# Kernel tuning notes

Hardware: AMD Instinct MI355X
Metric: run time of the kernel (lower is better)

The kernel has to match this reference:

```python
import jax, jax.numpy as jnp
import numpy as np

N, E, ET = 50000, 400000, 50000
F, ED, H, L = 64, 32, 128, 2


def _forward(x, edge_attr, target_edge_attr, node_W, node_b, edge_W, edge_b,
             pre_W, pre_b, post_W, post_b, lin_W, lin_b, bn_g, bn_b,
             em1_W, em1_b, em2_W, em2_b, edge_index):
    n = x.shape[0]
    h = node_W.shape[1]
    src, dst = edge_index[0], edge_index[1]
    x = x @ node_W + node_b                      # [N,H]
    ea = edge_attr @ edge_W + edge_b             # [E,H]
    tea = target_edge_attr @ edge_W + edge_b     # [Et,H]

    ones = jnp.ones((src.shape[0],), jnp.float32)
    cnt = jax.ops.segment_sum(ones, dst, num_segments=n)        # in-degree per node
    avg_deg_log = jnp.mean(jnp.log(cnt + 1.0))                  # PyG avg_deg['log'] from deg histogram
    deg = jnp.clip(cnt, 1.0)[:, None]
    amp = jnp.log(deg + 1.0) / avg_deg_log                      # 'amplification' scaler
    att = avg_deg_log / jnp.log(deg + 1.0)                      # 'attenuation' scaler
    cnt_c = jnp.clip(cnt, 1.0)[:, None]
    has = (cnt > 0)[:, None]

    nlayers = pre_W.shape[0]
    for i in range(nlayers):
        # pre-MLP on message cat([x_i(dst), x_j(src), edge_attr]); split matmul avoids [E,3H] concat
        Wd, Ws, We = pre_W[i, :h], pre_W[i, h:2 * h], pre_W[i, 2 * h:]
        m = x[dst] @ Wd + x[src] @ Ws + ea @ We + pre_b[i]      # [E,H]
        s = jax.ops.segment_sum(m, dst, num_segments=n)
        mean = s / cnt_c
        mean2 = jax.ops.segment_sum(m * m, dst, num_segments=n) / cnt_c
        std = jnp.sqrt(jax.nn.relu(mean2 - mean * mean) + 1e-5)  # PyG StdAggregation
        mn = jnp.where(has, jax.ops.segment_min(m, dst, num_segments=n), 0.0)
        mx = jnp.where(has, jax.ops.segment_max(m, dst, num_segments=n), 0.0)
        agg = jnp.concatenate([mean, mn, mx, std], axis=-1)     # [N,4H] aggregator order
        scaled = jnp.concatenate([agg, agg * amp, agg * att], axis=-1)  # [N,12H] scaler order
        # post-MLP on cat([x, scaled]); split matmul
        out = x @ post_W[i, :h] + scaled @ post_W[i, h:] + post_b[i]
        out = out @ lin_W[i] + lin_b[i]
        # BatchNorm (training mode, biased var, eps=1e-5)
        mu = out.mean(axis=0)
        var = jnp.mean((out - mu) ** 2, axis=0)
        bn = bn_g[i] * (out - mu) / jnp.sqrt(var + 1e-5) + bn_b[i]
        x = (x + jax.nn.relu(bn)) / 2
        # edge update: ea + MLP(cat([x[src], x[dst], ea])) / 2
        W1s, W1d, W1e = em1_W[i, :h], em1_W[i, h:2 * h], em1_W[i, 2 * h:]
        hid = jax.nn.relu(x[src] @ W1s + x[dst] @ W1d + ea @ W1e + em1_b[i])
        ea = ea + (hid @ em2_W[i] + em2_b[i]) / 2
    return (x, ea, tea)


def setup_inputs() -> dict:
    key = jax.random.key(0)
    ks = jax.random.split(key, 24)

    def w(k, shape):
        fan_in = shape[-2]
        return (jax.random.normal(k, shape, jnp.float32) / np.sqrt(fan_in)).astype(jnp.float32)

    inp = {
        'x': jax.random.normal(ks[0], (N, F), jnp.float32),
        'edge_attr': jax.random.normal(ks[1], (E, ED), jnp.float32),
        'target_edge_attr': jax.random.normal(ks[2], (ET, ED), jnp.float32),
        'node_W': w(ks[3], (F, H)), 'node_b': jnp.zeros((H,), jnp.float32),
        'edge_W': w(ks[4], (ED, H)), 'edge_b': jnp.zeros((H,), jnp.float32),
        'pre_W': w(ks[5], (L, 3 * H, H)), 'pre_b': jnp.zeros((L, H), jnp.float32),
        'post_W': w(ks[6], (L, 13 * H, H)), 'post_b': jnp.zeros((L, H), jnp.float32),
        'lin_W': w(ks[7], (L, H, H)), 'lin_b': jnp.zeros((L, H), jnp.float32),
        'bn_g': jnp.ones((L, H), jnp.float32), 'bn_b': jnp.zeros((L, H), jnp.float32),
        'em1_W': w(ks[8], (L, 3 * H, H)), 'em1_b': jnp.zeros((L, H), jnp.float32),
        'em2_W': w(ks[9], (L, H, H)), 'em2_b': jnp.zeros((L, H), jnp.float32),
        'edge_index': jax.random.randint(ks[10], (2, E), 0, N, dtype=jnp.int32),
    }
    return inp


def reference(x, edge_attr, target_edge_attr, node_W, node_b, edge_W, edge_b,
              pre_W, pre_b, post_W, post_b, lin_W, lin_b, bn_g, bn_b,
              em1_W, em1_b, em2_W, em2_b, edge_index):
    return _forward(x, edge_attr, target_edge_attr, node_W, node_b, edge_W, edge_b,
                    pre_W, pre_b, post_W, post_b, lin_W, lin_b, bn_g, bn_b,
                    em1_W, em1_b, em2_W, em2_b, edge_index)
```

## Files before the change

### kernel.cpp

```cpp
#include <hip/hip_runtime.h>
#include <math.h>

#define NN  50000
#define NE  400000
#define NTE 50000
#define FIN 64
#define EDIM 32
#define HD  128
#define NL  2
#define SCAN_B ((NN + 255) / 256)

typedef __attribute__((ext_vector_type(8))) short bf16x8;
typedef __attribute__((ext_vector_type(4))) short bf16x4;
typedef __attribute__((ext_vector_type(4))) float f32x4;

static __device__ __forceinline__ unsigned short f2bf(float f) {
    unsigned u = __float_as_uint(f);
    unsigned r = (u + 0x7fffu + ((u >> 16) & 1u)) >> 16;
    return (unsigned short)r;
}
static __device__ __forceinline__ float bfhi2f(unsigned u) { return __uint_as_float(u & 0xffff0000u); }
static __device__ __forceinline__ float bflo2f(unsigned u) { return __uint_as_float(u << 16); }

static __device__ __forceinline__ bf16x8 load_a8(const float* p, bool ok) {
    bf16x8 a = {};
    if (ok) {
        const float4 v0 = *(const float4*)(p);
        const float4 v1 = *(const float4*)(p + 4);
        a[0] = (short)f2bf(v0.x); a[1] = (short)f2bf(v0.y);
        a[2] = (short)f2bf(v0.z); a[3] = (short)f2bf(v0.w);
        a[4] = (short)f2bf(v1.x); a[5] = (short)f2bf(v1.y);
        a[6] = (short)f2bf(v1.z); a[7] = (short)f2bf(v1.w);
    }
    return a;
}
static __device__ __forceinline__ bf16x4 pack4(float4 a) {
    bf16x4 v;
    v[0]=(short)f2bf(a.x); v[1]=(short)f2bf(a.y); v[2]=(short)f2bf(a.z); v[3]=(short)f2bf(a.w);
    return v;
}
static __device__ __forceinline__ bf16x8 pack8(float4 a, float4 b) {
    bf16x8 v;
    v[0]=(short)f2bf(a.x); v[1]=(short)f2bf(a.y); v[2]=(short)f2bf(a.z); v[3]=(short)f2bf(a.w);
    v[4]=(short)f2bf(b.x); v[5]=(short)f2bf(b.y); v[6]=(short)f2bf(b.z); v[7]=(short)f2bf(b.w);
    return v;
}


__global__ void __launch_bounds__(256) k_packW(const float* __restrict__ W,
        unsigned short* __restrict__ out, int K)
{
    const int tid = blockIdx.x * 256 + threadIdx.x;
    const int total = (K / 32) * 512;
    if (tid >= total) return;
    const int lane = tid & 63, nt = (tid >> 6) & 7, kb = tid >> 9;
    const int k0 = kb * 32 + (lane >> 4) * 8;
    const int col = nt * 16 + (lane & 15);
    bf16x8 v;
    #pragma unroll
    for (int j = 0; j < 8; ++j)
        v[j] = (short)f2bf(W[(size_t)(k0 + j) * HD + col]);
    *(bf16x8*)(out + (size_t)tid * 8) = v;
}

__global__ void __launch_bounds__(256) k_foldW(const float* __restrict__ edgeW,
        const float* __restrict__ edgeb, const float* __restrict__ We0,
        float* __restrict__ Wf, float* __restrict__ bf)
{
    const int tid = blockIdx.x * 256 + threadIdx.x;
    if (tid < 4096) {
        const int k = tid >> 7, c = tid & 127;
        float s = 0.f;
        for (int j = 0; j < 128; ++j) s += edgeW[k * HD + j] * We0[(size_t)j * HD + c];
        Wf[tid] = s;
    } else if (tid < 4224) {
        const int c = tid - 4096;
        float s = 0.f;
        for (int j = 0; j < 128; ++j) s += edgeb[j] * We0[(size_t)j * HD + c];
        bf[c] = s;
    }
}

template<int KB>
__global__ void __launch_bounds__(256) k_gemm_T(const float* A,
        const unsigned short* __restrict__ Wpk, const float* __restrict__ bias,
        float* C, int M)
{
    const int t = threadIdx.x, w = t >> 6, l = t & 63;
    const int n = blockIdx.x * 64 + w * 16 + (l & 15);
    const bool ok = n < M;
    const int q = l >> 4;
    const int K = KB * 32;
    f32x4 acc[8] = {};
    #pragma unroll
    for (int kb = 0; kb < KB; ++kb) {
        const bf16x8 b = load_a8(A + (size_t)n * K + kb * 32 + q * 8, ok);
        #pragma unroll
        for (int nt = 0; nt < 8; ++nt) {
            const bf16x8 aW = *(const bf16x8*)(Wpk + (((size_t)(kb * 8 + nt) * 64 + l) << 3));
            acc[nt] = __builtin_amdgcn_mfma_f32_16x16x32_bf16(aW, b, acc[nt], 0, 0, 0);
        }
    }
    if (ok) {
        float* pc = C + (size_t)n * HD + q * 4;
        #pragma unroll
        for (int nt = 0; nt < 8; ++nt) {
            const int col = nt * 16 + q * 4;
            float4 bv = bias ? *(const float4*)(bias + col) : make_float4(0.f,0.f,0.f,0.f);
            float4 o;
            o.x = acc[nt][0] + bv.x; o.y = acc[nt][1] + bv.y;
            o.z = acc[nt][2] + bv.z; o.w = acc[nt][3] + bv.w;
            *(float4*)(pc + nt * 16) = o;
        }
    }
}

template<int KB>
__global__ void __launch_bounds__(256) k_gemm2_Tb(const float* A,
        const unsigned short* __restrict__ W0, const unsigned short* __restrict__ W1,
        const float* __restrict__ b0, unsigned short* C0, unsigned short* C1, int M)
{
    const int t = threadIdx.x, w = t >> 6, l = t & 63;
    const int n = blockIdx.x * 64 + w * 16 + (l & 15);
    const bool ok = n < M;
    const int q = l >> 4;
    const int K = KB * 32;
    f32x4 a0[8] = {}, a1[8] = {};
    #pragma unroll
    for (int kb = 0; kb < KB; ++kb) {
        const bf16x8 b = load_a8(A + (size_t)n * K + kb * 32 + q * 8, ok);
        #pragma unroll
        for (int nt = 0; nt < 8; ++nt) {
            const bf16x8 u = *(const bf16x8*)(W0 + (((size_t)(kb * 8 + nt) * 64 + l) << 3));
            const bf16x8 v = *(const bf16x8*)(W1 + (((size_t)(kb * 8 + nt) * 64 + l) << 3));
            a0[nt] = __builtin_amdgcn_mfma_f32_16x16x32_bf16(u, b, a0[nt], 0, 0, 0);
            a1[nt] = __builtin_amdgcn_mfma_f32_16x16x32_bf16(v, b, a1[nt], 0, 0, 0);
        }
    }
    if (ok) {
        unsigned short* p0 = C0 + (size_t)n * HD + q * 32;
        unsigned short* p1 = C1 + (size_t)n * HD + q * 32;
        #pragma unroll
        for (int k = 0; k < 4; ++k) {
            const int ntA = 2 * k, ntB = 2 * k + 1;
            float4 bA = b0 ? *(const float4*)(b0 + ntA * 16 + q * 4) : make_float4(0.f,0.f,0.f,0.f);
            float4 bB = b0 ? *(const float4*)(b0 + ntB * 16 + q * 4) : make_float4(0.f,0.f,0.f,0.f);
            float4 oA, oB;
            oA.x = a0[ntA][0]+bA.x; oA.y = a0[ntA][1]+bA.y; oA.z = a0[ntA][2]+bA.z; oA.w = a0[ntA][3]+bA.w;
            oB.x = a0[ntB][0]+bB.x; oB.y = a0[ntB][1]+bB.y; oB.z = a0[ntB][2]+bB.z; oB.w = a0[ntB][3]+bB.w;
            *(bf16x8*)(p0 + k * 8) = pack8(oA, oB);
            float4 uA = make_float4(a1[ntA][0], a1[ntA][1], a1[ntA][2], a1[ntA][3]);
            float4 uB = make_float4(a1[ntB][0], a1[ntB][1], a1[ntB][2], a1[ntB][3]);
            *(bf16x8*)(p1 + k * 8) = pack8(uA, uB);
        }
    }
}

__global__ void __launch_bounds__(256) k_count(const int* __restrict__ d, int* __restrict__ cnt, int E)
{
    const int e = blockIdx.x * 256 + threadIdx.x;
    if (e < E) atomicAdd(&cnt[d[e]], 1);
}

__global__ void __launch_bounds__(256) k_avglog(const int* __restrict__ cnt, float* __restrict__ stats)
{
    float s = 0.f;
    for (int n = blockIdx.x * 256 + threadIdx.x; n < NN; n += gridDim.x * 256)
        s += logf((float)cnt[n] + 1.f);
    #pragma unroll
    for (int off = 32; off > 0; off >>= 1) s += __shfl_down(s, off);
    __shared__ float ls[4];
    if ((threadIdx.x & 63) == 0) ls[threadIdx.x >> 6] = s;
    __syncthreads();
    if (threadIdx.x == 0) unsafeAtomicAdd(stats, ls[0] + ls[1] + ls[2] + ls[3]);
}

__global__ void __launch_bounds__(256) k_scan_block(const int* __restrict__ cnt,
        int* __restrict__ incl, int* __restrict__ part)
{
    __shared__ int s[256];
    const int t = threadIdx.x;
    const int i = blockIdx.x * 256 + t;
    const int v = (i < NN) ? cnt[i] : 0;
    s[t] = v;
    __syncthreads();
    #pragma unroll
    for (int off = 1; off < 256; off <<= 1) {
        const int x = (t >= off) ? s[t - off] : 0;
        __syncthreads();
        s[t] += x;
        __syncthreads();
    }
    if (i < NN) incl[i] = s[t];
    if (t == 255) part[blockIdx.x] = s[255];
}

__global__ void __launch_bounds__(256) k_scan_part(const int* __restrict__ part,
        int* __restrict__ poff, int np)
{
    __shared__ int s[256];
    const int t = threadIdx.x;
    const int v = (t < np) ? part[t] : 0;
    s[t] = v;
    __syncthreads();
    #pragma unroll
    for (int off = 1; off < 256; off <<= 1) {
        const int x = (t >= off) ? s[t - off] : 0;
        __syncthreads();
        s[t] += x;
        __syncthreads();
    }
    poff[t] = s[t] - v;
}

__global__ void __launch_bounds__(256) k_scan_add(const int* __restrict__ incl,
        const int* __restrict__ cnt, const int* __restrict__ poff,
        int* __restrict__ row_start, int* __restrict__ cursor)
{
    const int i = blockIdx.x * 256 + threadIdx.x;
    if (i < NN) {
        const int excl = incl[i] - cnt[i] + poff[blockIdx.x];
        row_start[i] = excl;
        cursor[i] = excl;
    }
    if (i == 0) row_start[NN] = NE;
}

__global__ void __launch_bounds__(256) k_scatter(const int* __restrict__ dstp,
        int* cursor, int* __restrict__ sppos)
{
    const int e = blockIdx.x * 256 + threadIdx.x;
    if (e < NE) sppos[e] = atomicAdd(&cursor[dstp[e]], 1);
}

template<int KB>
__global__ void __launch_bounds__(256) k_msg_T(const float* __restrict__ EA,
        const unsigned short* __restrict__ Wpk, const float* __restrict__ bias,
        const unsigned short* __restrict__ xsb, const int* __restrict__ srcp,
        const int* __restrict__ sppos, unsigned short* __restrict__ mbuf)
{
    const int t = threadIdx.x, w = t >> 6, l = t & 63;
    const int e = blockIdx.x * 64 + w * 16 + (l & 15);
    const int q = l >> 4;
    f32x4 acc[8] = {};
    #pragma unroll
    for (int kb = 0; kb < KB; ++kb) {
        const bf16x8 bea = load_a8(EA + (size_t)e * (KB * 32) + kb * 32 + q * 8, true);
        #pragma unroll
        for (int nt = 0; nt < 8; ++nt) {
            const bf16x8 aW = *(const bf16x8*)(Wpk + (((size_t)(kb * 8 + nt) * 64 + l) << 3));
            acc[nt] = __builtin_amdgcn_mfma_f32_16x16x32_bf16(aW, bea, acc[nt], 0, 0, 0);
        }
    }
    const int sn = srcp[e], sp = sppos[e];
    const unsigned short* ps = xsb + (size_t)sn * HD + q * 32;
    unsigned short* pm = mbuf + (size_t)sp * HD + q * 32;
    #pragma unroll
    for (int k = 0; k < 4; ++k) {
        const int ntA = 2 * k, ntB = 2 * k + 1;
        const uint4 su = *(const uint4*)(ps + k * 8);
        float4 oA, oB;
        oA.x = acc[ntA][0] + bflo2f(su.x); oA.y = acc[ntA][1] + bfhi2f(su.x);
        oA.z = acc[ntA][2] + bflo2f(su.y); oA.w = acc[ntA][3] + bfhi2f(su.y);
        oB.x = acc[ntB][0] + bflo2f(su.z); oB.y = acc[ntB][1] + bfhi2f(su.z);
        oB.z = acc[ntB][2] + bflo2f(su.w); oB.w = acc[ntB][3] + bfhi2f(su.w);
        if (bias) {
            const float4 bA = *(const float4*)(bias + ntA * 16 + q * 4);
            const float4 bB = *(const float4*)(bias + ntB * 16 + q * 4);
            oA.x += bA.x; oA.y += bA.y; oA.z += bA.z; oA.w += bA.w;
            oB.x += bB.x; oB.y += bB.y; oB.z += bB.z; oB.w += bB.w;
        }
        *(bf16x8*)(pm + k * 8) = pack8(oA, oB);
    }
}

__global__ void __launch_bounds__(256) k_agg(const unsigned short* __restrict__ mbuf,
        const int* __restrict__ rs, const unsigned short* __restrict__ xdb,
        const float* __restrict__ stats, unsigned short* __restrict__ aggb)
{
    const int n = blockIdx.x * 4 + (threadIdx.x >> 6);
    if (n >= NN) return;
    const int lane = threadIdx.x & 63;
    const int c = lane * 2;
    const int pidx = ((c & 12) << 3) + ((c >> 4) << 2) + (c & 3);
    const int s = rs[n], e = rs[n + 1];
    const unsigned xu = *(const unsigned*)(xdb + (size_t)n * HD + pidx);
    const float xv0 = bflo2f(xu), xv1 = bfhi2f(xu);
    float s0=0.f, s1=0.f, q0=0.f, q1=0.f;
    float mn0=INFINITY, mn1=INFINITY, mx0=-INFINITY, mx1=-INFINITY;
    for (int i = s; i < e; ++i) {
        const unsigned u = *(const unsigned*)(mbuf + (size_t)i * HD + pidx);
        const float v0 = bflo2f(u), v1 = bfhi2f(u);
        s0 += v0; s1 += v1;
        q0 += v0 * v0; q1 += v1 * v1;
        mn0 = fminf(mn0, v0); mn1 = fminf(mn1, v1);
        mx0 = fmaxf(mx0, v0); mx1 = fmaxf(mx1, v1);
    }
    const int deg = e - s;
    const float inv = 1.f / (float)(deg > 1 ? deg : 1);
    const float fd = (float)deg * inv;
    const float m0p = s0 * inv, m1p = s1 * inv;
    const float sd0 = sqrtf(fmaxf(q0 * inv - m0p * m0p, 0.f) + 1e-5f);
    const float sd1 = sqrtf(fmaxf(q1 * inv - m1p * m1p, 0.f) + 1e-5f);
    const bool has = deg > 0;
    const float v0[4] = { m0p + fd * xv0, has ? mn0 + xv0 : 0.f,
                          has ? mx0 + xv0 : 0.f, sd0 };
    const float v1[4] = { m1p + fd * xv1, has ? mn1 + xv1 : 0.f,
                          has ? mx1 + xv1 : 0.f, sd1 };
    const float avg = stats[0] * (1.f / (float)NN);
    const float lg = logf(fmaxf((float)deg, 1.f) + 1.f);
    const float amp = lg / avg, att = avg / lg;
    unsigned* a = (unsigned*)(aggb + (size_t)n * 1536 + c);
    #pragma unroll
    for (int sct = 0; sct < 4; ++sct) {
        a[sct * 64]       = (unsigned)f2bf(v0[sct])       | ((unsigned)f2bf(v1[sct]) << 16);
        a[256 + sct * 64] = (unsigned)f2bf(v0[sct] * amp) | ((unsigned)f2bf(v1[sct] * amp) << 16);
        a[512 + sct * 64] = (unsigned)f2bf(v0[sct] * att) | ((unsigned)f2bf(v1[sct] * att) << 16);
    }
}

__global__ void __launch_bounds__(256) k_post_lin_T(const float* __restrict__ x,
        const unsigned short* __restrict__ aggb, const unsigned short* __restrict__ PWpk,
        const float* __restrict__ pb, const unsigned short* __restrict__ LNpk,
        const float* __restrict__ lb, float* __restrict__ outb, int M)
{
    __shared__ unsigned short s_o16[64 * 128];
    const int t = threadIdx.x, w = t >> 6, l = t & 63;
    const int el = w * 16 + (l & 15);
    const int n = blockIdx.x * 64 + el;
    const bool ok = n < M;
    const int q = l >> 4;
    f32x4 acc[8] = {};
    #pragma unroll
    for (int kb = 0; kb < 4; ++kb) {
        const bf16x8 b = load_a8(x + (size_t)n * HD + kb * 32 + q * 8, ok);
        #pragma unroll
        for (int nt = 0; nt < 8; ++nt) {
            const bf16x8 aW = *(const bf16x8*)(PWpk + (((size_t)(kb * 8 + nt) * 64 + l) << 3));
            acc[nt] = __builtin_amdgcn_mfma_f32_16x16x32_bf16(aW, b, acc[nt], 0, 0, 0);
        }
    }
    const unsigned short* arow = aggb + (size_t)n * 1536 + q * 8;
    #pragma unroll 4
    for (int kb = 4; kb < 52; ++kb) {
        bf16x8 b = {};
        if (ok) b = *(const bf16x8*)(arow + (size_t)(kb - 4) * 32);
        #pragma unroll
        for (int nt = 0; nt < 8; ++nt) {
            const bf16x8 aW = *(const bf16x8*)(PWpk + (((size_t)(kb * 8 + nt) * 64 + l) << 3));
            acc[nt] = __builtin_amdgcn_mfma_f32_16x16x32_bf16(aW, b, acc[nt], 0, 0, 0);
        }
    }
    #pragma unroll
    for (int nt = 0; nt < 8; ++nt) {
        const int col = nt * 16 + q * 4;
        const float4 bv = *(const float4*)(pb + col);
        float4 o;
        o.x = acc[nt][0] + bv.x; o.y = acc[nt][1] + bv.y;
        o.z = acc[nt][2] + bv.z; o.w = acc[nt][3] + bv.w;
        const int bcol = nt * 32 + q * 8;
        const int slot = bcol >> 4;
        const int ba = el * 256 + ((slot ^ (el & 7)) << 4) + (bcol & 15);
        *(bf16x4*)((char*)s_o16 + ba) = pack4(o);
    }
    __syncthreads();
    f32x4 acc2[8] = {};
    #pragma unroll
    for (int kb = 0; kb < 4; ++kb) {
        const int slot = kb * 4 + q;
        const int ba = el * 256 + ((slot ^ (el & 7)) << 4);
        const bf16x8 bh = *(const bf16x8*)((const char*)s_o16 + ba);
        #pragma unroll
        for (int nt = 0; nt < 8; ++nt) {
            const bf16x8 aW = *(const bf16x8*)(LNpk + (((size_t)(kb * 8 + nt) * 64 + l) << 3));
            acc2[nt] = __builtin_amdgcn_mfma_f32_16x16x32_bf16(aW, bh, acc2[nt], 0, 0, 0);
        }
    }
    if (ok) {
        float* pc = outb + (size_t)n * HD + q * 4;
        #pragma unroll
        for (int nt = 0; nt < 8; ++nt) {
            const int col = nt * 16 + q * 4;
            const float4 bv = *(const float4*)(lb + col);
            float4 o;
            o.x = acc2[nt][0] + bv.x; o.y = acc2[nt][1] + bv.y;
            o.z = acc2[nt][2] + bv.z; o.w = acc2[nt][3] + bv.w;
            *(float4*)(pc + nt * 16) = o;
        }
    }
}

__global__ void __launch_bounds__(256) k_bnstats(const float* __restrict__ ob,
        float* __restrict__ bs, float* __restrict__ bq, int M)
{
    const int c = threadIdx.x & 127;
    const int gsub = threadIdx.x >> 7;
    float s = 0.f, qq = 0.f;
    for (int rr = blockIdx.x * 2 + gsub; rr < M; rr += gridDim.x * 2) {
        const float v = ob[(size_t)rr * HD + c];
        s += v; qq += v * v;
    }
    __shared__ float ls[2][HD], lq[2][HD];
    ls[gsub][c] = s; lq[gsub][c] = qq;
    __syncthreads();
    if (gsub == 0) {
        unsafeAtomicAdd(&bs[c], ls[0][c] + ls[1][c]);
        unsafeAtomicAdd(&bq[c], lq[0][c] + lq[1][c]);
    }
}

__global__ void __launch_bounds__(256) k_xupdate(float* x, const float* __restrict__ ob,
        const float* __restrict__ bs, const float* __restrict__ bq,
        const float* __restrict__ g, const float* __restrict__ bb)
{
    const int i = blockIdx.x * 256 + threadIdx.x;
    const int c0 = (i & 31) * 4;
    const float4 ov = ((const float4*)ob)[i];
    const float4 xv = ((const float4*)x)[i];
    const float o[4]  = {ov.x, ov.y, ov.z, ov.w};
    const float xo[4] = {xv.x, xv.y, xv.z, xv.w};
    float res[4];
    #pragma unroll
    for (int j = 0; j < 4; ++j) {
        const int c = c0 + j;
        const float mu  = bs[c] * (1.f / (float)NN);
        const float var = bq[c] * (1.f / (float)NN) - mu * mu;
        const float bn  = g[c] * (o[j] - mu) * rsqrtf(var + 1e-5f) + bb[c];
        res[j] = (xo[j] + fmaxf(bn, 0.f)) * 0.5f;
    }
    ((float4*)x)[i] = make_float4(res[0], res[1], res[2], res[3]);
}

__global__ void __launch_bounds__(256) k_edge_upd_T(float* ea,
        const unsigned short* __restrict__ W1epk, const unsigned short* __restrict__ e2pk,
        const float* __restrict__ e2b, const unsigned short* __restrict__ xs1b,
        const unsigned short* __restrict__ xd1b, const int* __restrict__ srcp,
        const int* __restrict__ dstp)
{
    __shared__ unsigned short s_hid[64 * 128];
    __shared__ float s_b2[128];
    const int t = threadIdx.x, w = t >> 6, l = t & 63;
    const int row0b = blockIdx.x * 64;
    if (t < 128) s_b2[t] = e2b[t];
    const int el = w * 16 + (l & 15);
    const int e = row0b + el;
    const int q = l >> 4, kq = q * 8;
    f32x4 acc1[8] = {};
    #pragma unroll
    for (int kb = 0; kb < 4; ++kb) {
        const bf16x8 bea = load_a8(ea + (size_t)e * HD + kb * 32 + kq, true);
        #pragma unroll
        for (int nt = 0; nt < 8; ++nt) {
            const bf16x8 aW = *(const bf16x8*)(W1epk + (((size_t)(kb * 8 + nt) * 64 + l) << 3));
            acc1[nt] = __builtin_amdgcn_mfma_f32_16x16x32_bf16(aW, bea, acc1[nt], 0, 0, 0);
        }
    }
    {
        const int sn = srcp[e], dn = dstp[e];
        const unsigned short* ps = xs1b + (size_t)sn * HD + q * 32;
        const unsigned short* pd = xd1b + (size_t)dn * HD + q * 32;
        #pragma unroll
        for (int k = 0; k < 4; ++k) {
            const int ntA = 2 * k, ntB = 2 * k + 1;
            const uint4 su = *(const uint4*)(ps + k * 8);
            const uint4 du = *(const uint4*)(pd + k * 8);
            float4 hA, hB;
            hA.x = fmaxf(acc1[ntA][0] + bflo2f(su.x) + bflo2f(du.x), 0.f);
            hA.y = fmaxf(acc1[ntA][1] + bfhi2f(su.x) + bfhi2f(du.x), 0.f);
            hA.z = fmaxf(acc1[ntA][2] + bflo2f(su.y) + bflo2f(du.y), 0.f);
            hA.w = fmaxf(acc1[ntA][3] + bfhi2f(su.y) + bfhi2f(du.y), 0.f);
            hB.x = fmaxf(acc1[ntB][0] + bflo2f(su.z) + bflo2f(du.z), 0.f);
            hB.y = fmaxf(acc1[ntB][1] + bfhi2f(su.z) + bfhi2f(du.z), 0.f);
            hB.z = fmaxf(acc1[ntB][2] + bflo2f(su.w) + bflo2f(du.w), 0.f);
            hB.w = fmaxf(acc1[ntB][3] + bfhi2f(su.w) + bfhi2f(du.w), 0.f);
            const int bcolA = ntA * 32 + q * 8;
            const int baA = el * 256 + (((bcolA >> 4) ^ (el & 7)) << 4) + (bcolA & 15);
            *(bf16x4*)((char*)s_hid + baA) = pack4(hA);
            const int bcolB = ntB * 32 + q * 8;
            const int baB = el * 256 + (((bcolB >> 4) ^ (el & 7)) << 4) + (bcolB & 15);
            *(bf16x4*)((char*)s_hid + baB) = pack4(hB);
        }
    }
    __syncthreads();
    f32x4 acc2[8] = {};
    #pragma unroll
    for (int kb = 0; kb < 4; ++kb) {
        const int slot = kb * 4 + q;
        const int ba = el * 256 + ((slot ^ (el & 7)) << 4);
        const bf16x8 bh = *(const bf16x8*)((const char*)s_hid + ba);
        #pragma unroll
        for (int nt = 0; nt < 8; ++nt) {
            const bf16x8 aW = *(const bf16x8*)(e2pk + (((size_t)(kb * 8 + nt) * 64 + l) << 3));
            acc2[nt] = __builtin_amdgcn_mfma_f32_16x16x32_bf16(aW, bh, acc2[nt], 0, 0, 0);
        }
    }
    {
        float* pe = ea + (size_t)e * HD + q * 4;
        #pragma unroll
        for (int nt = 0; nt < 8; ++nt) {
            const float4 eo = *(const float4*)(pe + nt * 16);
            const float4 bv = *(const float4*)(&s_b2[nt * 16 + q * 4]);
            float4 o;
            o.x = eo.x + (acc2[nt][0] + bv.x) * 0.5f;
            o.y = eo.y + (acc2[nt][1] + bv.y) * 0.5f;
            o.z = eo.z + (acc2[nt][2] + bv.z) * 0.5f;
            o.w = eo.w + (acc2[nt][3] + bv.w) * 0.5f;
            *(float4*)(pe + nt * 16) = o;
        }
    }
}

extern "C" void kernel_launch(void* const* d_in, const int* in_sizes, int n_in,
                              void* d_out, int out_size, void* d_ws, size_t ws_size,
                              hipStream_t stream)
{
    const float* x0    = (const float*)d_in[0];
    const float* eatr  = (const float*)d_in[1];
    const float* teatr = (const float*)d_in[2];
    const float* nodeW = (const float*)d_in[3];
    const float* nodeb = (const float*)d_in[4];
    const float* edgeW = (const float*)d_in[5];
    const float* edgeb = (const float*)d_in[6];
    const float* preW  = (const float*)d_in[7];
    const float* preb  = (const float*)d_in[8];
    const float* postW = (const float*)d_in[9];
    const float* postb = (const float*)d_in[10];
    const float* linW  = (const float*)d_in[11];
    const float* linb  = (const float*)d_in[12];
    const float* bng   = (const float*)d_in[13];
    const float* bnb   = (const float*)d_in[14];
    const float* em1W  = (const float*)d_in[15];
    const float* em1b  = (const float*)d_in[16];
    const float* em2W  = (const float*)d_in[17];
    const float* em2b  = (const float*)d_in[18];
    const int*   eidx  = (const int*)d_in[19];
    const int* srcp = eidx;
    const int* dstp = eidx + NE;

    float* out_x  = (float*)d_out;
    float* out_ea = out_x + (size_t)NN * HD;
    float* out_te = out_ea + (size_t)NE * HD;

    const size_t NH = (size_t)NN * HD;
    const size_t EH = (size_t)NE * HD;
    unsigned short* xdb = (unsigned short*)d_ws;
    unsigned short* xsb = xdb + NH;
    float* outb  = (float*)(xsb + NH);
    float* stats = outb + NH;
    float* Wf    = stats + 512;
    float* bfold = Wf + 4096;
    int*   cnt      = (int*)(bfold + 128);
    int*   row_start = cnt + NN;
    int*   cursor   = row_start + NN + 1;
    int*   tmpincl  = cursor + NN;
    int*   part     = tmpincl + NN;
    int*   poff     = part + 256;
    int*   sppos    = poff + 256;
    unsigned short* mbuf = (unsigned short*)(((uintptr_t)(sppos + NE) + 15) & ~(uintptr_t)15);
    unsigned short* aggb = mbuf + EH;
    unsigned short* pk   = aggb + (size_t)NN * 1536;
    const size_t KBSZ = 512 * 8;
    unsigned short* pkPost = pk;
    unsigned short* pkPre  = pkPost + 104 * KBSZ;
    unsigned short* pkEm1  = pkPre  + 24 * KBSZ;
    unsigned short* pkLin  = pkEm1  + 24 * KBSZ;
    unsigned short* pkEm2  = pkLin  + 8 * KBSZ;
    unsigned short* pkNode = pkEm2  + 8 * KBSZ;
    unsigned short* pkEdge = pkNode + 2 * KBSZ;
    unsigned short* pkWe0f = pkEdge + 1 * KBSZ;

    hipMemsetAsync(cnt, 0, NN * sizeof(int), stream);
    hipMemsetAsync(stats, 0, 512 * sizeof(float), stream);

    k_packW<<<208, 256, 0, stream>>>(postW, pkPost, 3328);
    k_packW<<<48, 256, 0, stream>>>(preW,  pkPre,  768);
    k_packW<<<48, 256, 0, stream>>>(em1W,  pkEm1,  768);
    k_packW<<<16, 256, 0, stream>>>(linW,  pkLin,  256);
    k_packW<<<16, 256, 0, stream>>>(em2W,  pkEm2,  256);
    k_packW<<<4, 256, 0, stream>>>(nodeW, pkNode, 64);
    k_packW<<<2, 256, 0, stream>>>(edgeW, pkEdge, 32);
    k_foldW<<<17, 256, 0, stream>>>(edgeW, edgeb, preW + 256 * HD, Wf, bfold);
    k_packW<<<2, 256, 0, stream>>>(Wf, pkWe0f, 32);

    k_gemm_T<1><<<(NE + 63) / 64, 256, 0, stream>>>(eatr, pkEdge, edgeb, out_ea, NE);
    k_gemm_T<1><<<(NTE + 63) / 64, 256, 0, stream>>>(teatr, pkEdge, edgeb, out_te, NTE);
    k_gemm_T<2><<<(NN + 63) / 64, 256, 0, stream>>>(x0, pkNode, nodeb, out_x, NN);

    k_count<<<(NE + 255) / 256, 256, 0, stream>>>(dstp, cnt, NE);
    k_avglog<<<256, 256, 0, stream>>>(cnt, stats);
    k_scan_block<<<SCAN_B, 256, 0, stream>>>(cnt, tmpincl, part);
    k_scan_part<<<1, 256, 0, stream>>>(part, poff, SCAN_B);
    k_scan_add<<<SCAN_B, 256, 0, stream>>>(tmpincl, cnt, poff, row_start, cursor);
    k_scatter<<<(NE + 255) / 256, 256, 0, stream>>>(dstp, cursor, sppos);

    const int gn = (NN + 63) / 64;
    const int ge = NE / 64;

    for (int l = 0; l < NL; ++l) {
        const unsigned short* Wd_pk  = pkPre + (size_t)(l * 12 + 0) * KBSZ;
        const unsigned short* Ws_pk  = pkPre + (size_t)(l * 12 + 4) * KBSZ;
        const unsigned short* We_pk  = pkPre + (size_t)(l * 12 + 8) * KBSZ;
        const unsigned short* W1s_pk = pkEm1 + (size_t)(l * 12 + 0) * KBSZ;
        const unsigned short* W1d_pk = pkEm1 + (size_t)(l * 12 + 4) * KBSZ;
        const unsigned short* W1e_pk = pkEm1 + (size_t)(l * 12 + 8) * KBSZ;
        const unsigned short* PW_pk  = pkPost + (size_t)l * 52 * KBSZ;
        const unsigned short* lin_pk = pkLin + (size_t)l * 4 * KBSZ;
        const unsigned short* em2_pk = pkEm2 + (size_t)l * 4 * KBSZ;
        const float* pbl = preb + l * HD;
        const float* pob = postb + l * HD;
        const float* lb  = linb + l * HD;
        const float* g_  = bng + l * HD;
        const float* b_  = bnb + l * HD;
        const float* e1b = em1b + l * HD;
        const float* e2b = em2b + l * HD;

        hipMemsetAsync(stats + 128, 0, 256 * sizeof(float), stream);

        k_gemm2_Tb<4><<<gn, 256, 0, stream>>>(out_x, Wd_pk, Ws_pk, pbl, xdb, xsb, NN);
        if (l == 0)
            k_msg_T<1><<<ge, 256, 0, stream>>>(eatr, pkWe0f, bfold, xsb, srcp, sppos, mbuf);
        else
            k_msg_T<4><<<ge, 256, 0, stream>>>(out_ea, We_pk, nullptr, xsb, srcp, sppos, mbuf);
        k_agg<<<(NN + 3) / 4, 256, 0, stream>>>(mbuf, row_start, xdb, stats, aggb);
        k_post_lin_T<<<gn, 256, 0, stream>>>(out_x, aggb, PW_pk, pob, lin_pk, lb, outb, NN);
        k_bnstats<<<256, 256, 0, stream>>>(outb, stats + 128, stats + 256, NN);
        k_xupdate<<<NN * 32 / 256, 256, 0, stream>>>(out_x, outb, stats + 128, stats + 256, g_, b_);
        k_gemm2_Tb<4><<<gn, 256, 0, stream>>>(out_x, W1d_pk, W1s_pk, e1b, xdb, xsb, NN);
        k_edge_upd_T<<<ge, 256, 0, stream>>>(out_ea, W1e_pk, em2_pk, e2b, xsb, xdb, srcp, dstp);
    }
}
```

Measured before the change: 1.438 ms.

## Fold edge embedding into layer-0 edge update and skip initial edge GEMM

Drops the separate edge-embedding GEMM that wrote the E×H edge features. Layer 0's edge update now recomputes the embedding from the raw 32-dim edge attributes through MFMA. It also folds edge_W into the em1 edge weight slice, so the first MLP takes the 32-dim input directly. This removes one full E×128 fp32 write and the later read of it, but adds extra MFMA work and two small folding kernels. The embedding now goes through bf16 for the residual term, which may change precision slightly.

```diff
diff --git a/kernel.cpp b/kernel.cpp
--- a/kernel.cpp
+++ b/kernel.cpp
@@ -64,19 +64,19 @@
 }
 
 __global__ void __launch_bounds__(256) k_foldW(const float* __restrict__ edgeW,
-        const float* __restrict__ edgeb, const float* __restrict__ We0,
+        const float* __restrict__ edgeb, const float* __restrict__ W,
         float* __restrict__ Wf, float* __restrict__ bf)
 {
     const int tid = blockIdx.x * 256 + threadIdx.x;
     if (tid < 4096) {
         const int k = tid >> 7, c = tid & 127;
         float s = 0.f;
-        for (int j = 0; j < 128; ++j) s += edgeW[k * HD + j] * We0[(size_t)j * HD + c];
+        for (int j = 0; j < 128; ++j) s += edgeW[k * HD + j] * W[(size_t)j * HD + c];
         Wf[tid] = s;
     } else if (tid < 4224) {
         const int c = tid - 4096;
         float s = 0.f;
-        for (int j = 0; j < 128; ++j) s += edgeb[j] * We0[(size_t)j * HD + c];
+        for (int j = 0; j < 128; ++j) s += edgeb[j] * W[(size_t)j * HD + c];
         bf[c] = s;
     }
 }
@@ -429,6 +429,88 @@
         res[j] = (xo[j] + fmaxf(bn, 0.f)) * 0.5f;
     }
     ((float4*)x)[i] = make_float4(res[0], res[1], res[2], res[3]);
+}
+
+__global__ void __launch_bounds__(256) k_edge_upd0_T(const float* __restrict__ eatr,
+        float* __restrict__ ea,
+        const unsigned short* __restrict__ edgepk, const float* __restrict__ edgeb,
+        const unsigned short* __restrict__ Wf1pk, const float* __restrict__ bf1,
+        const unsigned short* __restrict__ e2pk, const float* __restrict__ e2b,
+        const unsigned short* __restrict__ xs1b, const unsigned short* __restrict__ xd1b,
+        const int* __restrict__ srcp, const int* __restrict__ dstp)
+{
+    __shared__ unsigned short s_hid[64 * 128];
+    __shared__ float s_b2[128];
+    const int t = threadIdx.x, w = t >> 6, l = t & 63;
+    if (t < 128) s_b2[t] = e2b[t];
+    const int el = w * 16 + (l & 15);
+    const int e = blockIdx.x * 64 + el;
+    const int q = l >> 4;
+    const int sn = srcp[e], dn = dstp[e];
+    const bf16x8 bet = load_a8(eatr + (size_t)e * EDIM + q * 8, true);
+    f32x4 ea0[8] = {}, hp[8] = {};
+    #pragma unroll
+    for (int nt = 0; nt < 8; ++nt) {
+        const bf16x8 aE = *(const bf16x8*)(edgepk + (((size_t)nt * 64 + l) << 3));
+        const bf16x8 aF = *(const bf16x8*)(Wf1pk + (((size_t)nt * 64 + l) << 3));
+        ea0[nt] = __builtin_amdgcn_mfma_f32_16x16x32_bf16(aE, bet, ea0[nt], 0, 0, 0);
+        hp[nt]  = __builtin_amdgcn_mfma_f32_16x16x32_bf16(aF, bet, hp[nt], 0, 0, 0);
+    }
+    {
+        const unsigned short* ps = xs1b + (size_t)sn * HD + q * 32;
+        const unsigned short* pd = xd1b + (size_t)dn * HD + q * 32;
+        #pragma unroll
+        for (int k = 0; k < 4; ++k) {
+            const int ntA = 2 * k, ntB = 2 * k + 1;
+            const uint4 su = *(const uint4*)(ps + k * 8);
+            const uint4 du = *(const uint4*)(pd + k * 8);
+            const float4 bA = *(const float4*)(bf1 + ntA * 16 + q * 4);
+            const float4 bB = *(const float4*)(bf1 + ntB * 16 + q * 4);
+            float4 hA, hB;
+            hA.x = fmaxf(hp[ntA][0] + bA.x + bflo2f(su.x) + bflo2f(du.x), 0.f);
+            hA.y = fmaxf(hp[ntA][1] + bA.y + bfhi2f(su.x) + bfhi2f(du.x), 0.f);
+            hA.z = fmaxf(hp[ntA][2] + bA.z + bflo2f(su.y) + bflo2f(du.y), 0.f);
+            hA.w = fmaxf(hp[ntA][3] + bA.w + bfhi2f(su.y) + bfhi2f(du.y), 0.f);
+            hB.x = fmaxf(hp[ntB][0] + bB.x + bflo2f(su.z) + bflo2f(du.z), 0.f);
+            hB.y = fmaxf(hp[ntB][1] + bB.y + bfhi2f(su.z) + bfhi2f(du.z), 0.f);
+            hB.z = fmaxf(hp[ntB][2] + bB.z + bflo2f(su.w) + bflo2f(du.w), 0.f);
+            hB.w = fmaxf(hp[ntB][3] + bB.w + bfhi2f(su.w) + bfhi2f(du.w), 0.f);
+            const int bcolA = ntA * 32 + q * 8;
+            const int baA = el * 256 + (((bcolA >> 4) ^ (el & 7)) << 4) + (bcolA & 15);
+            *(bf16x4*)((char*)s_hid + baA) = pack4(hA);
+            const int bcolB = ntB * 32 + q * 8;
+            const int baB = el * 256 + (((bcolB >> 4) ^ (el & 7)) << 4) + (bcolB & 15);
+            *(bf16x4*)((char*)s_hid + baB) = pack4(hB);
+        }
+    }
+    __syncthreads();
+    f32x4 acc2[8] = {};
+    #pragma unroll
+    for (int kb = 0; kb < 4; ++kb) {
+        const int slot = kb * 4 + q;
+        const int ba = el * 256 + ((slot ^ (el & 7)) << 4);
+        const bf16x8 bh = *(const bf16x8*)((const char*)s_hid + ba);
+        #pragma unroll
+        for (int nt = 0; nt < 8; ++nt) {
+            const bf16x8 aW = *(const bf16x8*)(e2pk + (((size_t)(kb * 8 + nt) * 64 + l) << 3));
+            acc2[nt] = __builtin_amdgcn_mfma_f32_16x16x32_bf16(aW, bh, acc2[nt], 0, 0, 0);
+        }
+    }
+    {
+        float* pe = ea + (size_t)e * HD + q * 4;
+        #pragma unroll
+        for (int nt = 0; nt < 8; ++nt) {
+            const int col = nt * 16 + q * 4;
+            const float4 eb = *(const float4*)(edgeb + col);
+            const float4 bv = *(const float4*)(&s_b2[col]);
+            float4 o;
+            o.x = ea0[nt][0] + eb.x + (acc2[nt][0] + bv.x) * 0.5f;
+            o.y = ea0[nt][1] + eb.y + (acc2[nt][1] + bv.y) * 0.5f;
+            o.z = ea0[nt][2] + eb.z + (acc2[nt][2] + bv.z) * 0.5f;
+            o.w = ea0[nt][3] + eb.w + (acc2[nt][3] + bv.w) * 0.5f;
+            *(float4*)(pe + nt * 16) = o;
+        }
+    }
 }
 
 __global__ void __launch_bounds__(256) k_edge_upd_T(float* ea,
@@ -547,9 +629,11 @@
     unsigned short* xsb = xdb + NH;
     float* outb  = (float*)(xsb + NH);
     float* stats = outb + NH;
-    float* Wf    = stats + 512;
-    float* bfold = Wf + 4096;
-    int*   cnt      = (int*)(bfold + 128);
+    float* Wf0   = stats + 512;
+    float* bf0   = Wf0 + 4096;
+    float* Wf1   = bf0 + 128;
+    float* bf1   = Wf1 + 4096;
+    int*   cnt      = (int*)(bf1 + 128);
     int*   row_start = cnt + NN;
     int*   cursor   = row_start + NN + 1;
     int*   tmpincl  = cursor + NN;
@@ -568,6 +652,7 @@
     unsigned short* pkNode = pkEm2  + 8 * KBSZ;
     unsigned short* pkEdge = pkNode + 2 * KBSZ;
     unsigned short* pkWe0f = pkEdge + 1 * KBSZ;
+    unsigned short* pkWf1  = pkWe0f + 1 * KBSZ;
 
     hipMemsetAsync(cnt, 0, NN * sizeof(int), stream);
     hipMemsetAsync(stats, 0, 512 * sizeof(float), stream);
@@ -579,10 +664,11 @@
     k_packW<<<16, 256, 0, stream>>>(em2W,  pkEm2,  256);
     k_packW<<<4, 256, 0, stream>>>(nodeW, pkNode, 64);
     k_packW<<<2, 256, 0, stream>>>(edgeW, pkEdge, 32);
-    k_foldW<<<17, 256, 0, stream>>>(edgeW, edgeb, preW + 256 * HD, Wf, bfold);
-    k_packW<<<2, 256, 0, stream>>>(Wf, pkWe0f, 32);
-
-    k_gemm_T<1><<<(NE + 63) / 64, 256, 0, stream>>>(eatr, pkEdge, edgeb, out_ea, NE);
+    k_foldW<<<17, 256, 0, stream>>>(edgeW, edgeb, preW + 256 * HD, Wf0, bf0);
+    k_foldW<<<17, 256, 0, stream>>>(edgeW, edgeb, em1W + 256 * HD, Wf1, bf1);
+    k_packW<<<2, 256, 0, stream>>>(Wf0, pkWe0f, 32);
+    k_packW<<<2, 256, 0, stream>>>(Wf1, pkWf1, 32);
+
     k_gemm_T<1><<<(NTE + 63) / 64, 256, 0, stream>>>(teatr, pkEdge, edgeb, out_te, NTE);
     k_gemm_T<2><<<(NN + 63) / 64, 256, 0, stream>>>(x0, pkNode, nodeb, out_x, NN);
 
@@ -618,7 +704,7 @@
 
         k_gemm2_Tb<4><<<gn, 256, 0, stream>>>(out_x, Wd_pk, Ws_pk, pbl, xdb, xsb, NN);
         if (l == 0)
-            k_msg_T<1><<<ge, 256, 0, stream>>>(eatr, pkWe0f, bfold, xsb, srcp, sppos, mbuf);
+            k_msg_T<1><<<ge, 256, 0, stream>>>(eatr, pkWe0f, bf0, xsb, srcp, sppos, mbuf);
         else
             k_msg_T<4><<<ge, 256, 0, stream>>>(out_ea, We_pk, nullptr, xsb, srcp, sppos, mbuf);
         k_agg<<<(NN + 3) / 4, 256, 0, stream>>>(mbuf, row_start, xdb, stats, aggb);
@@ -626,6 +712,10 @@
         k_bnstats<<<256, 256, 0, stream>>>(outb, stats + 128, stats + 256, NN);
         k_xupdate<<<NN * 32 / 256, 256, 0, stream>>>(out_x, outb, stats + 128, stats + 256, g_, b_);
         k_gemm2_Tb<4><<<gn, 256, 0, stream>>>(out_x, W1d_pk, W1s_pk, e1b, xdb, xsb, NN);
-        k_edge_upd_T<<<ge, 256, 0, stream>>>(out_ea, W1e_pk, em2_pk, e2b, xsb, xdb, srcp, dstp);
-    }
-}
+        if (l == 0)
+            k_edge_upd0_T<<<ge, 256, 0, stream>>>(eatr, out_ea, pkEdge, edgeb,
+                                                  pkWf1, bf1, em2_pk, e2b, xsb, xdb, srcp, dstp);
+        else
+            k_edge_upd_T<<<ge, 256, 0, stream>>>(out_ea, W1e_pk, em2_pk, e2b, xsb, xdb, srcp, dstp);
+    }
+}
```

Result: faster. 1.334 ms (-7.2%).
